# Optimization experiments

Measured on AMD Instinct MI355X. Metric: run time of the kernel, lower is better.

Reference implementation:

```python
import jax, jax.numpy as jnp
import numpy as np

SCALE = 0.2  # init_kwargs: scale
EPS = 1e-12  # F.normalize default eps


def setup_inputs() -> dict:
    key = jax.random.key(0)
    x = jax.random.normal(key, (8, 2048, 512), dtype=jnp.float32)
    return {"x": x}


def reference(x):
    # x: [B, N, D]
    # F.normalize(x, dim=2): x / max(||x||_2, eps)
    norm = jnp.linalg.norm(x, axis=2, keepdims=True)
    x_norm = x / jnp.maximum(norm, EPS)
    # sim: [B, N, N] = x_norm @ x_norm^T, softmax over last dim
    sim = jnp.einsum('bnd,bmd->bnm', x_norm, x_norm)
    attn = jax.nn.softmax(sim, axis=2)
    # (1 + scale) * x - scale * attn @ x
    out = (1.0 + SCALE) * x - SCALE * jnp.einsum('bnm,bmd->bnd', attn, x)
    return out
```

## Files before the change

kernel.cpp:

```cpp
#include <hip/hip_runtime.h>
#include <stdint.h>

typedef unsigned short ushort_t;
typedef float f32x2 __attribute__((ext_vector_type(2)));
typedef float f32x4 __attribute__((ext_vector_type(4)));
typedef float f32x16 __attribute__((ext_vector_type(16)));
typedef short bf16x8 __attribute__((ext_vector_type(8)));
typedef unsigned short us8 __attribute__((ext_vector_type(8)));

#define BATCH 8
#define SEQ   2048
#define DIM   512
#define KBLK  64
#define NIT   (SEQ / KBLK)
#define LDS_TOTAL 156160

__device__ __forceinline__ ushort_t f2bf(float f) {
  union { float f; uint32_t u; } c; c.f = f;
  uint32_t u = c.u;
  return (ushort_t)((u + 0x7FFFu + ((u >> 16) & 1u)) >> 16);
}
__device__ __forceinline__ uint32_t packbf(float a, float b) {
  return (uint32_t)f2bf(a) | ((uint32_t)f2bf(b) << 16);
}
__device__ __forceinline__ void gload_lds16(const void* g, void* l) {
  __builtin_amdgcn_global_load_lds(
      (const __attribute__((address_space(1))) unsigned int*)g,
      (__attribute__((address_space(3))) unsigned int*)l, 16, 0, 0);
}
#define WAIT_LGKM_BAR() { asm volatile("s_waitcnt lgkmcnt(0)" ::: "memory"); \
  __builtin_amdgcn_s_barrier(); __builtin_amdgcn_sched_barrier(0); }
#define WAIT_ALL_BAR()  { asm volatile("s_waitcnt vmcnt(0) lgkmcnt(0)" ::: "memory"); \
  __builtin_amdgcn_s_barrier(); __builtin_amdgcn_sched_barrier(0); }

__global__ void k_prep(const float* __restrict__ x, ushort_t* __restrict__ xn,
                       ushort_t* __restrict__ vt) {
  __shared__ __align__(16) ushort_t tile[64][512];
  const int tid = threadIdx.x, lane = tid & 63, w = tid >> 6;
  const int b = blockIdx.x >> 5, nt = blockIdx.x & 31;
  const size_t row0 = (size_t)b * SEQ + (size_t)nt * 64;

  for (int j = 0; j < 16; ++j) {
    const int r = w * 16 + j;
    const float* xr = x + (row0 + r) * DIM;
    const float4 a  = ((const float4*)xr)[lane * 2];
    const float4 bb = ((const float4*)xr)[lane * 2 + 1];
    float ss = a.x*a.x + a.y*a.y + a.z*a.z + a.w*a.w
             + bb.x*bb.x + bb.y*bb.y + bb.z*bb.z + bb.w*bb.w;
#pragma unroll
    for (int m = 32; m >= 1; m >>= 1) ss += __shfl_xor(ss, m, 64);
    const float rn = 1.2011224087864498f / sqrtf(fmaxf(ss, 1e-24f));
    us8 nrm, raw;
    nrm[0]=f2bf(a.x*rn);  nrm[1]=f2bf(a.y*rn);  nrm[2]=f2bf(a.z*rn);  nrm[3]=f2bf(a.w*rn);
    nrm[4]=f2bf(bb.x*rn); nrm[5]=f2bf(bb.y*rn); nrm[6]=f2bf(bb.z*rn); nrm[7]=f2bf(bb.w*rn);
    raw[0]=f2bf(a.x);  raw[1]=f2bf(a.y);  raw[2]=f2bf(a.z);  raw[3]=f2bf(a.w);
    raw[4]=f2bf(bb.x); raw[5]=f2bf(bb.y); raw[6]=f2bf(bb.z); raw[7]=f2bf(bb.w);
    *(us8*)(xn + (row0 + r) * DIM + lane * 8) = nrm;
    *(us8*)(&tile[r][lane * 8]) = raw;
  }
  __syncthreads();
#pragma unroll
  for (int pass = 0; pass < 2; ++pass) {
    const int d = pass * 256 + tid;
    ushort_t* dst = vt + ((size_t)b * DIM + d) * SEQ + (size_t)nt * 64;
#pragma unroll
    for (int g = 0; g < 8; ++g) {
      us8 v;
#pragma unroll
      for (int e = 0; e < 8; ++e) v[e] = tile[g * 8 + e][d];
      *(us8*)(dst + g * 8) = v;
    }
  }
}

__launch_bounds__(512, 2)
__global__ void k_attn(const ushort_t* __restrict__ xn, const ushort_t* __restrict__ vt,
                       const float* __restrict__ x, float* __restrict__ out) {
  extern __shared__ char smem[];
  char* const Kb0 = smem;
  char* const Kb1 = smem + 65536;
  ushort_t* const P = (ushort_t*)(smem + 131072);
  float* const Sp   = (float*)(smem + 139264);
  float* const lsum = (float*)(smem + 155648);

  const int tid = threadIdx.x;
  const int lane = tid & 63, w = tid >> 6;
  const int kw = w & 1, qw = (w >> 1) & 1, kd = w >> 2;
  const int l31 = lane & 31, l5 = lane >> 5, l7 = lane & 7;
  const int b = blockIdx.x & 7, qt0 = blockIdx.x >> 3;
  const int q0 = qt0 * 64;

  const ushort_t* xnb = xn + (size_t)b * SEQ * DIM;
  const ushort_t* vtb = vt + (size_t)b * DIM * SEQ;

  bf16x8 qreg[16];
#pragma unroll
  for (int ks = 0; ks < 16; ++ks)
    qreg[ks] = *(const bf16x8*)(xnb + (size_t)(q0 + qw * 32 + l31) * DIM
                                + kd * 256 + ks * 16 + l5 * 8);

  f32x16 acc[2][2] = {};
  float plsum = 0.f;

#pragma unroll
  for (int i = 0; i < 8; ++i) {
    const int row = w * 8 + i;
    gload_lds16(xnb + (size_t)row * DIM + ((lane ^ i) << 3), Kb0 + row * 1024);
  }
  asm volatile("s_waitcnt vmcnt(0)" ::: "memory");
  __builtin_amdgcn_s_barrier();
  __builtin_amdgcn_sched_barrier(0);

  for (int t = 0; t < NIT; ++t) {
    const int k0 = t * KBLK;
    char* const Kc = (t & 1) ? Kb1 : Kb0;
    char* const Kn = (t & 1) ? Kb0 : Kb1;

    f32x16 accS = {};
    const int arow = kw * 32 + l31;
#pragma unroll
    for (int ks = 0; ks < 16; ++ks) {
      const int c = kd * 32 + ks * 2 + l5;
      bf16x8 af = *(const bf16x8*)(Kc + arow * 1024 + ((c ^ l7) << 4));
      accS = __builtin_amdgcn_mfma_f32_32x32x16_bf16(af, qreg[ks], accS, 0, 0, 0);
    }

    if (kd) {
      float* tile = Sp + (kw * 2 + qw) * 1024 + l31 * 32;
#pragma unroll
      for (int j = 0; j < 8; ++j) {
        const int u = (j & 1) + 4 * (j >> 1) + 2 * l5;
        f32x2 v = { accS[2 * j], accS[2 * j + 1] };
        *(f32x2*)(tile + ((u ^ l7) << 1)) = v;
      }
    }
    WAIT_LGKM_BAR();

    bf16x8 vv[2][4];
#pragma unroll
    for (int dt = 0; dt < 2; ++dt)
#pragma unroll
      for (int ks = 0; ks < 4; ++ks)
        vv[dt][ks] = *(const bf16x8*)(vtb + (size_t)(w * 64 + dt * 32 + l31) * SEQ
                                      + k0 + ks * 16 + l5 * 8);

    if (!kd) {
      const float* tile = Sp + (kw * 2 + qw) * 1024 + l31 * 32;
      uint32_t* prow = (uint32_t*)(P + (qw * 32 + l31) * 64);
#pragma unroll
      for (int j = 0; j < 8; ++j) {
        const int u = (j & 1) + 4 * (j >> 1) + 2 * l5;
        f32x2 o = *(const f32x2*)(tile + ((u ^ l7) << 1));
        float p0 = __builtin_amdgcn_exp2f(accS[2 * j]     + o[0]);
        float p1 = __builtin_amdgcn_exp2f(accS[2 * j + 1] + o[1]);
        plsum += p0 + p1;
        const int chunk = (kw * 4 + (j >> 1)) ^ l7;
        prow[chunk * 4 + (j & 1) + 2 * l5] = packbf(p0, p1);
      }
    } else if (t + 1 < NIT) {
      const int sid = w - 4;
#pragma unroll
      for (int i = 0; i < 16; ++i) {
        const int row = sid * 16 + i;
        gload_lds16(xnb + (size_t)(k0 + KBLK + row) * DIM + ((lane ^ (i & 7)) << 3),
                    Kn + row * 1024);
      }
    }
    WAIT_LGKM_BAR();

#pragma unroll
    for (int qt = 0; qt < 2; ++qt) {
#pragma unroll
      for (int ks = 0; ks < 4; ++ks) {
        const int c = (ks * 2 + l5) ^ l7;
        bf16x8 pa = *(const bf16x8*)(P + (qt * 32 + l31) * 64 + c * 8);
        acc[qt][0] = __builtin_amdgcn_mfma_f32_32x32x16_bf16(pa, vv[0][ks], acc[qt][0], 0, 0, 0);
        acc[qt][1] = __builtin_amdgcn_mfma_f32_32x32x16_bf16(pa, vv[1][ks], acc[qt][1], 0, 0, 0);
      }
    }
    WAIT_ALL_BAR();
  }

  if (!kd) {
    plsum += __shfl_xor(plsum, 32, 64);
    if (lane < 32) lsum[kw * 64 + qw * 32 + lane] = plsum;
  }
  float* obuf = (float*)smem;
#pragma unroll
  for (int qt = 0; qt < 2; ++qt)
#pragma unroll
    for (int dt = 0; dt < 2; ++dt) {
      const int d = w * 64 + dt * 32 + l31;
#pragma unroll
      for (int r = 0; r < 16; ++r) {
        const int q = qt * 32 + (r & 3) + 8 * (r >> 2) + 4 * l5;
        const int c = (d >> 2) ^ (q & 7);
        obuf[q * 512 + c * 4 + (d & 3)] = acc[qt][dt][r];
      }
    }
  WAIT_LGKM_BAR();

  const int q = tid >> 3, seg = tid & 7;
  const float s = 0.2f / (lsum[q] + lsum[64 + q]);
  const size_t grow = ((size_t)b * SEQ + q0 + q) * DIM;
#pragma unroll
  for (int i = 0; i < 16; ++i) {
    const int c = seg * 16 + i;
    const int cs = c ^ (q & 7);
    f32x4 a = *(const f32x4*)(obuf + q * 512 + cs * 4);
    const float4 xv = *(const float4*)(x + grow + c * 4);
    float4 o;
    o.x = 1.2f * xv.x - s * a[0];
    o.y = 1.2f * xv.y - s * a[1];
    o.z = 1.2f * xv.z - s * a[2];
    o.w = 1.2f * xv.w - s * a[3];
    *(float4*)(out + grow + c * 4) = o;
  }
}

extern "C" void kernel_launch(void* const* d_in, const int* in_sizes, int n_in,
                              void* d_out, int out_size, void* d_ws, size_t ws_size,
                              hipStream_t stream) {
  const float* x = (const float*)d_in[0];
  float* out = (float*)d_out;
  ushort_t* xn = (ushort_t*)d_ws;
  ushort_t* vt = (ushort_t*)((char*)d_ws + (size_t)BATCH * SEQ * DIM * 2);

  k_prep<<<BATCH * (SEQ / 64), 256, 0, stream>>>(x, xn, vt);
  (void)hipFuncSetAttribute((const void*)k_attn,
                            hipFuncAttributeMaxDynamicSharedMemorySize, LDS_TOTAL);
  k_attn<<<BATCH * SEQ / 64, 512, LDS_TOTAL, stream>>>(xn, vt, x, out);
}
```

Baseline: 226.4 us.

## Reuse normalized K tile as V via LDS transpose reads, dropping separate V transpose

```diff
diff --git a/kernel.cpp b/kernel.cpp
--- a/kernel.cpp
+++ b/kernel.cpp
@@ -2,18 +2,21 @@
 #include <stdint.h>
 
 typedef unsigned short ushort_t;
+typedef unsigned int u32x2 __attribute__((ext_vector_type(2)));
 typedef float f32x2 __attribute__((ext_vector_type(2)));
 typedef float f32x4 __attribute__((ext_vector_type(4)));
 typedef float f32x16 __attribute__((ext_vector_type(16)));
 typedef short bf16x8 __attribute__((ext_vector_type(8)));
 typedef unsigned short us8 __attribute__((ext_vector_type(8)));
 
+#define AS3 __attribute__((address_space(3)))
+
 #define BATCH 8
 #define SEQ   2048
 #define DIM   512
 #define KBLK  64
 #define NIT   (SEQ / KBLK)
-#define LDS_TOTAL 156160
+#define LDS_TOTAL 155648
 
 __device__ __forceinline__ ushort_t f2bf(float f) {
   union { float f; uint32_t u; } c; c.f = f;
@@ -25,8 +28,9 @@
 }
 __device__ __forceinline__ void gload_lds16(const void* g, void* l) {
   __builtin_amdgcn_global_load_lds(
-      (const __attribute__((address_space(1))) unsigned int*)g,
-      (__attribute__((address_space(3))) unsigned int*)l, 16, 0, 0);
+      (const AS3 unsigned int*)0 == 0 ? (const __attribute__((address_space(1))) unsigned int*)g
+                                      : (const __attribute__((address_space(1))) unsigned int*)g,
+      (AS3 unsigned int*)l, 16, 0, 0);
 }
 #define WAIT_LGKM_BAR() { asm volatile("s_waitcnt lgkmcnt(0)" ::: "memory"); \
   __builtin_amdgcn_s_barrier(); __builtin_amdgcn_sched_barrier(0); }
@@ -34,64 +38,45 @@
   __builtin_amdgcn_s_barrier(); __builtin_amdgcn_sched_barrier(0); }
 
 __global__ void k_prep(const float* __restrict__ x, ushort_t* __restrict__ xn,
-                       ushort_t* __restrict__ vt) {
-  __shared__ __align__(16) ushort_t tile[64][512];
-  const int tid = threadIdx.x, lane = tid & 63, w = tid >> 6;
-  const int b = blockIdx.x >> 5, nt = blockIdx.x & 31;
-  const size_t row0 = (size_t)b * SEQ + (size_t)nt * 64;
-
-  for (int j = 0; j < 16; ++j) {
-    const int r = w * 16 + j;
-    const float* xr = x + (row0 + r) * DIM;
-    const float4 a  = ((const float4*)xr)[lane * 2];
-    const float4 bb = ((const float4*)xr)[lane * 2 + 1];
-    float ss = a.x*a.x + a.y*a.y + a.z*a.z + a.w*a.w
-             + bb.x*bb.x + bb.y*bb.y + bb.z*bb.z + bb.w*bb.w;
-#pragma unroll
-    for (int m = 32; m >= 1; m >>= 1) ss += __shfl_xor(ss, m, 64);
-    const float rn = 1.2011224087864498f / sqrtf(fmaxf(ss, 1e-24f));
-    us8 nrm, raw;
-    nrm[0]=f2bf(a.x*rn);  nrm[1]=f2bf(a.y*rn);  nrm[2]=f2bf(a.z*rn);  nrm[3]=f2bf(a.w*rn);
-    nrm[4]=f2bf(bb.x*rn); nrm[5]=f2bf(bb.y*rn); nrm[6]=f2bf(bb.z*rn); nrm[7]=f2bf(bb.w*rn);
-    raw[0]=f2bf(a.x);  raw[1]=f2bf(a.y);  raw[2]=f2bf(a.z);  raw[3]=f2bf(a.w);
-    raw[4]=f2bf(bb.x); raw[5]=f2bf(bb.y); raw[6]=f2bf(bb.z); raw[7]=f2bf(bb.w);
-    *(us8*)(xn + (row0 + r) * DIM + lane * 8) = nrm;
-    *(us8*)(&tile[r][lane * 8]) = raw;
-  }
-  __syncthreads();
-#pragma unroll
-  for (int pass = 0; pass < 2; ++pass) {
-    const int d = pass * 256 + tid;
-    ushort_t* dst = vt + ((size_t)b * DIM + d) * SEQ + (size_t)nt * 64;
-#pragma unroll
-    for (int g = 0; g < 8; ++g) {
-      us8 v;
-#pragma unroll
-      for (int e = 0; e < 8; ++e) v[e] = tile[g * 8 + e][d];
-      *(us8*)(dst + g * 8) = v;
-    }
-  }
-}
-
-__launch_bounds__(512, 2)
-__global__ void k_attn(const ushort_t* __restrict__ xn, const ushort_t* __restrict__ vt,
-                       const float* __restrict__ x, float* __restrict__ out) {
+                       float* __restrict__ irn) {
+  const int lane = threadIdx.x & 63;
+  const int w    = threadIdx.x >> 6;
+  const size_t row = (size_t)blockIdx.x * 4 + w;
+  const float* xr = x + row * DIM;
+  const float4 a = ((const float4*)xr)[lane * 2];
+  const float4 b = ((const float4*)xr)[lane * 2 + 1];
+  float ss = a.x*a.x + a.y*a.y + a.z*a.z + a.w*a.w
+           + b.x*b.x + b.y*b.y + b.z*b.z + b.w*b.w;
+#pragma unroll
+  for (int m = 32; m >= 1; m >>= 1) ss += __shfl_xor(ss, m, 64);
+  const float nrm2 = sqrtf(fmaxf(ss, 1e-24f));
+  const float rn = 1.2011224087864498f / nrm2;
+  us8 o;
+  o[0] = f2bf(a.x*rn); o[1] = f2bf(a.y*rn); o[2] = f2bf(a.z*rn); o[3] = f2bf(a.w*rn);
+  o[4] = f2bf(b.x*rn); o[5] = f2bf(b.y*rn); o[6] = f2bf(b.z*rn); o[7] = f2bf(b.w*rn);
+  *(us8*)(xn + row * DIM + lane * 8) = o;
+  if (lane == 0) irn[row] = nrm2 / 1.2011224087864498f;
+}
+
+__global__ __launch_bounds__(512, 2)
+void k_attn(const ushort_t* __restrict__ xn, const float* __restrict__ irn,
+            const float* __restrict__ x, float* __restrict__ out) {
   extern __shared__ char smem[];
   char* const Kb0 = smem;
   char* const Kb1 = smem + 65536;
-  ushort_t* const P = (ushort_t*)(smem + 131072);
-  float* const Sp   = (float*)(smem + 139264);
-  float* const lsum = (float*)(smem + 155648);
+  char* const Pl  = smem + 131072;
+  float* const Sp = (float*)(smem + 139264);
+  float* const lsum = (float*)(smem + 139264);
 
   const int tid = threadIdx.x;
   const int lane = tid & 63, w = tid >> 6;
   const int kw = w & 1, qw = (w >> 1) & 1, kd = w >> 2;
-  const int l31 = lane & 31, l5 = lane >> 5, l7 = lane & 7;
+  const int l31 = lane & 31, l5 = lane >> 5;
   const int b = blockIdx.x & 7, qt0 = blockIdx.x >> 3;
   const int q0 = qt0 * 64;
 
   const ushort_t* xnb = xn + (size_t)b * SEQ * DIM;
-  const ushort_t* vtb = vt + (size_t)b * DIM * SEQ;
+  const float*    irb = irn + (size_t)b * SEQ;
 
   bf16x8 qreg[16];
 #pragma unroll
@@ -102,11 +87,23 @@
   f32x16 acc[2][2] = {};
   float plsum = 0.f;
 
-#pragma unroll
-  for (int i = 0; i < 8; ++i) {
-    const int row = w * 8 + i;
-    gload_lds16(xnb + (size_t)row * DIM + ((lane ^ i) << 3), Kb0 + row * 1024);
-  }
+  const int kblkA = (kw * 32 + l31) >> 2, kinA = (kw * 32 + l31) & 3;
+  const int fb = kd * 8;
+  const int wb = (kd ^ 1) * 8;
+  const int slotW = ((kw * 2 + qw) * 2 + kd);
+  const int slotR = ((kw * 2 + qw) * 2 + (kd ^ 1));
+
+  auto stage = [&](int k0, char* Kb) {
+#pragma unroll
+    for (int i = 0; i < 8; ++i) {
+      const int c = i * 512 + tid;
+      const int k = ((c >> 8) << 2) + ((c >> 1) & 3);
+      const int dblk = (c >> 3) & 31, dh = c & 1;
+      gload_lds16(xnb + (size_t)(k0 + k) * DIM + dblk * 16 + dh * 8, Kb + c * 16);
+    }
+  };
+
+  stage(0, Kb0);
   asm volatile("s_waitcnt vmcnt(0)" ::: "memory");
   __builtin_amdgcn_s_barrier();
   __builtin_amdgcn_sched_barrier(0);
@@ -115,76 +112,71 @@
     const int k0 = t * KBLK;
     char* const Kc = (t & 1) ? Kb1 : Kb0;
     char* const Kn = (t & 1) ? Kb0 : Kb1;
+    const uint kcb = (uint)(uintptr_t)(AS3 char*)Kc;
+
+    if (t + 1 < NIT) stage(k0 + KBLK, Kn);
+    const f32x4 i0 = *(const f32x4*)(irb + k0 + kw * 32 + kd * 16 + 4 * l5);
+    const f32x4 i1 = *(const f32x4*)(irb + k0 + kw * 32 + kd * 16 + 4 * l5 + 8);
 
     f32x16 accS = {};
-    const int arow = kw * 32 + l31;
 #pragma unroll
     for (int ks = 0; ks < 16; ++ks) {
-      const int c = kd * 32 + ks * 2 + l5;
-      bf16x8 af = *(const bf16x8*)(Kc + arow * 1024 + ((c ^ l7) << 4));
+      const bf16x8 af = *(const bf16x8*)(Kc + (((kblkA * 32 + kd * 16 + ks) << 7)
+                                               + (kinA << 5) + (l5 << 4)));
       accS = __builtin_amdgcn_mfma_f32_32x32x16_bf16(af, qreg[ks], accS, 0, 0, 0);
     }
 
-    if (kd) {
-      float* tile = Sp + (kw * 2 + qw) * 1024 + l31 * 32;
-#pragma unroll
-      for (int j = 0; j < 8; ++j) {
-        const int u = (j & 1) + 4 * (j >> 1) + 2 * l5;
-        f32x2 v = { accS[2 * j], accS[2 * j + 1] };
-        *(f32x2*)(tile + ((u ^ l7) << 1)) = v;
+#pragma unroll
+    for (int p = 0; p < 4; ++p) {
+      f32x2 v = { accS[wb + 2 * p], accS[wb + 2 * p + 1] };
+      *(f32x2*)(Sp + ((slotW * 4 + p) * 2 + l5) * 64 + l31 * 2) = v;
+    }
+    WAIT_LGKM_BAR();
+
+    const float ir[8] = { i0[0], i0[1], i0[2], i0[3], i1[0], i1[1], i1[2], i1[3] };
+    uint32_t* prow = (uint32_t*)(Pl + (size_t)(qw * 32 + l31) * 128);
+#pragma unroll
+    for (int p = 0; p < 4; ++p) {
+      const f32x2 o = *(const f32x2*)(Sp + ((slotR * 4 + p) * 2 + l5) * 64 + l31 * 2);
+      const float e0 = __builtin_amdgcn_exp2f(accS[fb + 2 * p]     + o[0]);
+      const float e1 = __builtin_amdgcn_exp2f(accS[fb + 2 * p + 1] + o[1]);
+      plsum += e0 + e1;
+      const int chunk = (kw * 4 + kd * 2 + (p >> 1)) ^ (l31 & 7);
+      prow[chunk * 4 + (p & 1) + 2 * l5] = packbf(e0 * ir[2 * p], e1 * ir[2 * p + 1]);
+    }
+    WAIT_LGKM_BAR();
+
+#pragma unroll
+    for (int ks = 0; ks < 4; ++ks) {
+      const bf16x8 pa0 = *(const bf16x8*)(Pl + (size_t)(0 * 32 + l31) * 128
+                                          + ((((ks * 2 + l5) ^ (l31 & 7))) << 4));
+      const bf16x8 pa1 = *(const bf16x8*)(Pl + (size_t)(1 * 32 + l31) * 128
+                                          + ((((ks * 2 + l5) ^ (l31 & 7))) << 4));
+      union { u32x2 u[2]; bf16x8 v; } B0, B1;
+      const int kblk1 = ks * 4 + l5 * 2;
+      {
+        const uint a0 = kcb + (((kblk1 * 32 + (w * 4 + 0 * 2 + (l31 >> 4))) << 7)
+                               + ((l31 & 15) << 3));
+        asm volatile("ds_read_b64_tr_b16 %0, %1" : "=v"(B0.u[0]) : "v"(a0));
+        asm volatile("ds_read_b64_tr_b16 %0, %1 offset:4096" : "=v"(B0.u[1]) : "v"(a0));
+        const uint a1 = kcb + (((kblk1 * 32 + (w * 4 + 1 * 2 + (l31 >> 4))) << 7)
+                               + ((l31 & 15) << 3));
+        asm volatile("ds_read_b64_tr_b16 %0, %1" : "=v"(B1.u[0]) : "v"(a1));
+        asm volatile("ds_read_b64_tr_b16 %0, %1 offset:4096" : "=v"(B1.u[1]) : "v"(a1));
       }
-    }
-    WAIT_LGKM_BAR();
-
-    bf16x8 vv[2][4];
-#pragma unroll
-    for (int dt = 0; dt < 2; ++dt)
-#pragma unroll
-      for (int ks = 0; ks < 4; ++ks)
-        vv[dt][ks] = *(const bf16x8*)(vtb + (size_t)(w * 64 + dt * 32 + l31) * SEQ
-                                      + k0 + ks * 16 + l5 * 8);
-
-    if (!kd) {
-      const float* tile = Sp + (kw * 2 + qw) * 1024 + l31 * 32;
-      uint32_t* prow = (uint32_t*)(P + (qw * 32 + l31) * 64);
-#pragma unroll
-      for (int j = 0; j < 8; ++j) {
-        const int u = (j & 1) + 4 * (j >> 1) + 2 * l5;
-        f32x2 o = *(const f32x2*)(tile + ((u ^ l7) << 1));
-        float p0 = __builtin_amdgcn_exp2f(accS[2 * j]     + o[0]);
-        float p1 = __builtin_amdgcn_exp2f(accS[2 * j + 1] + o[1]);
-        plsum += p0 + p1;
-        const int chunk = (kw * 4 + (j >> 1)) ^ l7;
-        prow[chunk * 4 + (j & 1) + 2 * l5] = packbf(p0, p1);
-      }
-    } else if (t + 1 < NIT) {
-      const int sid = w - 4;
-#pragma unroll
-      for (int i = 0; i < 16; ++i) {
-        const int row = sid * 16 + i;
-        gload_lds16(xnb + (size_t)(k0 + KBLK + row) * DIM + ((lane ^ (i & 7)) << 3),
-                    Kn + row * 1024);
-      }
-    }
-    WAIT_LGKM_BAR();
-
-#pragma unroll
-    for (int qt = 0; qt < 2; ++qt) {
-#pragma unroll
-      for (int ks = 0; ks < 4; ++ks) {
-        const int c = (ks * 2 + l5) ^ l7;
-        bf16x8 pa = *(const bf16x8*)(P + (qt * 32 + l31) * 64 + c * 8);
-        acc[qt][0] = __builtin_amdgcn_mfma_f32_32x32x16_bf16(pa, vv[0][ks], acc[qt][0], 0, 0, 0);
-        acc[qt][1] = __builtin_amdgcn_mfma_f32_32x32x16_bf16(pa, vv[1][ks], acc[qt][1], 0, 0, 0);
-      }
+      asm volatile("s_waitcnt lgkmcnt(0)" ::: "memory");
+      __builtin_amdgcn_sched_barrier(0);
+      acc[0][0] = __builtin_amdgcn_mfma_f32_32x32x16_bf16(pa0, B0.v, acc[0][0], 0, 0, 0);
+      acc[0][1] = __builtin_amdgcn_mfma_f32_32x32x16_bf16(pa0, B1.v, acc[0][1], 0, 0, 0);
+      acc[1][0] = __builtin_amdgcn_mfma_f32_32x32x16_bf16(pa1, B0.v, acc[1][0], 0, 0, 0);
+      acc[1][1] = __builtin_amdgcn_mfma_f32_32x32x16_bf16(pa1, B1.v, acc[1][1], 0, 0, 0);
     }
     WAIT_ALL_BAR();
   }
 
-  if (!kd) {
-    plsum += __shfl_xor(plsum, 32, 64);
-    if (lane < 32) lsum[kw * 64 + qw * 32 + lane] = plsum;
-  }
+  plsum += __shfl_xor(plsum, 32, 64);
+  if (lane < 32) lsum[(kw * 2 + kd) * 64 + qw * 32 + l31] = plsum;
+
   float* obuf = (float*)smem;
 #pragma unroll
   for (int qt = 0; qt < 2; ++qt)
@@ -201,7 +193,7 @@
   WAIT_LGKM_BAR();
 
   const int q = tid >> 3, seg = tid & 7;
-  const float s = 0.2f / (lsum[q] + lsum[64 + q]);
+  const float s = 0.2f / (lsum[q] + lsum[64 + q] + lsum[128 + q] + lsum[192 + q]);
   const size_t grow = ((size_t)b * SEQ + q0 + q) * DIM;
 #pragma unroll
   for (int i = 0; i < 16; ++i) {
@@ -224,10 +216,10 @@
   const float* x = (const float*)d_in[0];
   float* out = (float*)d_out;
   ushort_t* xn = (ushort_t*)d_ws;
-  ushort_t* vt = (ushort_t*)((char*)d_ws + (size_t)BATCH * SEQ * DIM * 2);
-
-  k_prep<<<BATCH * (SEQ / 64), 256, 0, stream>>>(x, xn, vt);
+  float* irn = (float*)((char*)d_ws + (size_t)BATCH * SEQ * DIM * 2);
+
+  k_prep<<<BATCH * SEQ / 4, 256, 0, stream>>>(x, xn, irn);
   (void)hipFuncSetAttribute((const void*)k_attn,
                             hipFuncAttributeMaxDynamicSharedMemorySize, LDS_TOTAL);
-  k_attn<<<BATCH * SEQ / 64, 512, LDS_TOTAL, stream>>>(xn, vt, x, out);
-}
+  k_attn<<<BATCH * SEQ / 64, 512, LDS_TOTAL, stream>>>(xn, irn, x, out);
+}
```

Result: no change. 222.0 us (-1.9%).
